# Performance work log

Measured on AMD Instinct MI355X. Metric: run time of the kernel, lower is better.

The kernel has to match this reference:

```python
import jax, jax.numpy as jnp
import numpy as np

B, S, D, H, BU = 64, 1024, 256, 512, 512  # batch, seq_len, input_size, units, backbone width


def setup_inputs() -> dict:
    key = jax.random.key(0)
    k0, k1, k2, k3 = jax.random.split(key, 4)
    inputs = jax.random.normal(k0, (B, S, D), dtype=jnp.float32)
    # backbone: Linear(D+H -> BU) (single layer, no trailing activation per build_backbone)
    Wb = jax.random.normal(k1, (D + H, BU), dtype=jnp.float32) * 0.02
    bb = jnp.zeros((BU,), dtype=jnp.float32)
    # head: Linear(BU -> H)
    Wh = jax.random.normal(k2, (BU, H), dtype=jnp.float32) * 0.02
    bh = jnp.zeros((H,), dtype=jnp.float32)
    # per-unit liquid time constant tau > 0
    tau = 1.0 + jax.random.uniform(k3, (H,), dtype=jnp.float32)
    return {"inputs": inputs, "Wb": Wb, "bb": bb, "Wh": Wh, "bh": bh, "tau": tau}


def reference(inputs, Wb, bb, Wh, bh, tau):
    # LiquidRNN: unidirectional, return_sequences=True, zero initial state, dt=1.0
    dt = jnp.float32(1.0)
    batch = inputs.shape[0]
    h0 = jnp.zeros((batch, Wh.shape[1]), dtype=inputs.dtype)

    def step(h, x):  # x: [B, D], h: [B, H]
        z = jnp.concatenate([x, h], axis=-1) @ Wb + bb          # backbone [B, BU]
        d = jnp.tanh(z @ Wh + bh)                               # target activation [B, H]
        h_new = h + dt * (d - h) / tau                          # liquid ODE (Euler) update
        return h_new, h_new

    _, outs = jax.lax.scan(step, h0, jnp.swapaxes(inputs, 0, 1))  # outs: [S, B, H]
    return jnp.swapaxes(outs, 0, 1)  # [B, S, H]
```

## Files before the change

### kernel.cpp

```cpp
#include <hip/hip_runtime.h>
#include <hip/hip_bf16.h>


#define S_   1024
#define D_   256
#define H_   512
#define KT_  768
#define NKC_ 24

typedef __attribute__((ext_vector_type(4))) float f32x4;
typedef __attribute__((ext_vector_type(8))) short bf16x8;
typedef unsigned long long u64;

static __device__ __forceinline__ unsigned short f2bf(float f) {
    unsigned int x = __float_as_uint(f);
    return (unsigned short)((x + 0x7fffu + ((x >> 16) & 1u)) >> 16);
}

__global__ void k_prep(const float* __restrict__ Wb, const float* __restrict__ bb,
                       const float* __restrict__ Wh, const float* __restrict__ bh,
                       const float* __restrict__ tau,
                       unsigned short* __restrict__ Mfrag, float* __restrict__ c,
                       float* __restrict__ itau, unsigned* __restrict__ hz) {
    int i = blockIdx.x * 256 + threadIdx.x;
    if (i < KT_ * H_) {
        int r = i >> 9, n = i & 511;
        float acc = 0.f;
        for (int u = 0; u < 512; ++u)
            acc += Wb[r * 512 + u] * Wh[u * 512 + n];
        int kc   = r >> 5;
        int j    = r & 7;
        int lane = (((r >> 3) & 3) << 4) | (n & 15);
        int nt   = n >> 4;
        Mfrag[((nt * NKC_ + kc) * 64 + lane) * 8 + j] = f2bf(acc);
    } else if (i < KT_ * H_ + 512) {
        int n = i - KT_ * H_;
        float acc = bh[n];
        for (int u = 0; u < 512; ++u)
            acc += bb[u] * Wh[u * 512 + n];
        c[n] = acc;
    } else if (i < KT_ * H_ + 1024) {
        itau[i - KT_ * H_ - 512] = 1.0f / tau[i - KT_ * H_ - 512];
    } else {
        int z = i - KT_ * H_ - 1024;
        if (z < 65536) hz[z] = 0u;
    }
}

__global__ __launch_bounds__(256, 1)
void k_rnn2(const float* __restrict__ x, const unsigned short* __restrict__ Mfrag,
            const float* __restrict__ c, const float* __restrict__ itau,
            u64* __restrict__ hb, float* __restrict__ out) {
    const int g    = blockIdx.x >> 3;
    const int s    = blockIdx.x & 7;
    const int tid  = threadIdx.x;
    const int w    = tid >> 6;
    const int lane = tid & 63;
    const int quad = lane >> 4;
    const int m16  = lane & 15;
    const int nt   = s * 4 + w;
    const int C0   = nt * 16 + quad * 4;
    const int b    = g * 16 + m16;

    const bf16x8* Mf = reinterpret_cast<const bf16x8*>(Mfrag);
    bf16x8 wreg[NKC_];
#pragma unroll
    for (int kc = 0; kc < NKC_; ++kc)
        wreg[kc] = Mf[(nt * NKC_ + kc) * 64 + lane];

    const f32x4 cs = *reinterpret_cast<const f32x4*>(c + C0);
    const f32x4 ts = *reinterpret_cast<const f32x4*>(itau + C0);

    const int jsel = quad & 1;
    const int st_u = ((C0 >> 3) * 16 + m16) * 4 + jsel * 2;
    const int ld_u = lane * 4;

    f32x4 h_old = {0.f, 0.f, 0.f, 0.f};

    for (int t = 0; t < S_; ++t) {
        const float* xp = x + ((size_t)b * S_ + t) * D_ + quad * 8;
        f32x4 xa[8], xb[8];
#pragma unroll
        for (int kc = 0; kc < 8; ++kc) {
            xa[kc] = *reinterpret_cast<const f32x4*>(xp + kc * 32);
            xb[kc] = *reinterpret_cast<const f32x4*>(xp + kc * 32 + 4);
        }
        f32x4 a0 = {0.f, 0.f, 0.f, 0.f}, a1 = {0.f, 0.f, 0.f, 0.f};
#pragma unroll
        for (int kc = 0; kc < 8; ++kc) {
            bf16x8 xv;
#pragma unroll
            for (int j = 0; j < 4; ++j) {
                xv[j]     = (short)f2bf(xa[kc][j]);
                xv[j + 4] = (short)f2bf(xb[kc][j]);
            }
            if (kc & 1) a1 = __builtin_amdgcn_mfma_f32_16x16x32_bf16(wreg[kc], xv, a1, 0, 0, 0);
            else        a0 = __builtin_amdgcn_mfma_f32_16x16x32_bf16(wreg[kc], xv, a0, 0, 0, 0);
        }

        if (t > 0) {
            u64* hbl = hb + (size_t)(g * 2 + (t & 1)) * 4096;
            u64 hl[16][4];
#pragma unroll
            for (int kc = 0; kc < 16; ++kc) {
#pragma unroll
                for (int q = 0; q < 4; ++q)
                    hl[kc][q] = __hip_atomic_load(hbl + kc * 256 + ld_u + q,
                                                  __ATOMIC_RELAXED, __HIP_MEMORY_SCOPE_AGENT);
            }
            const unsigned T = (unsigned)t << 16;
            for (;;) {
                unsigned bad = 0u;
#pragma unroll
                for (int kc = 0; kc < 16; ++kc) {
#pragma unroll
                    for (int q = 0; q < 4; ++q) {
                        unsigned lo = (unsigned)hl[kc][q];
                        unsigned hi = (unsigned)(hl[kc][q] >> 32);
                        bad |= (lo ^ T) | (hi ^ T);
                    }
                }
                if (!__any((bad & 0xFFFF0000u) != 0u)) break;
#pragma unroll
                for (int kc = 0; kc < 16; ++kc) {
#pragma unroll
                    for (int q = 0; q < 4; ++q)
                        hl[kc][q] = __hip_atomic_load(hbl + kc * 256 + ld_u + q,
                                                      __ATOMIC_RELAXED, __HIP_MEMORY_SCOPE_AGENT);
                }
            }
#pragma unroll
            for (int kc = 0; kc < 16; ++kc) {
                union { unsigned wv[4]; bf16x8 v; } hv;
#pragma unroll
                for (int q = 0; q < 4; ++q) {
                    unsigned lo = (unsigned)hl[kc][q];
                    unsigned hi = (unsigned)(hl[kc][q] >> 32);
                    hv.wv[q] = (lo & 0xffffu) | (hi << 16);
                }
                if (kc & 1) a1 = __builtin_amdgcn_mfma_f32_16x16x32_bf16(wreg[8 + kc], hv.v, a1, 0, 0, 0);
                else        a0 = __builtin_amdgcn_mfma_f32_16x16x32_bf16(wreg[8 + kc], hv.v, a0, 0, 0, 0);
            }
        }

        f32x4 acc = a0 + a1;
        f32x4 hn;
        unsigned dv[4];
        const unsigned Tn = (unsigned)(t + 1) << 16;
#pragma unroll
        for (int r = 0; r < 4; ++r) {
            float u = acc[r] + cs[r];
            float e = __expf(2.f * u);
            float d = 1.f - 2.f / (e + 1.f);
            hn[r] = h_old[r] + (d - h_old[r]) * ts[r];
            dv[r] = (unsigned)f2bf(hn[r]) | Tn;
        }
        h_old = hn;

        u64 p0 = (u64)dv[0] | ((u64)dv[1] << 32);
        u64 p1 = (u64)dv[2] | ((u64)dv[3] << 32);
        u64* hbs = hb + (size_t)(g * 2 + ((t + 1) & 1)) * 4096;
        __hip_atomic_store(hbs + st_u,     p0, __ATOMIC_RELAXED, __HIP_MEMORY_SCOPE_AGENT);
        __hip_atomic_store(hbs + st_u + 1, p1, __ATOMIC_RELAXED, __HIP_MEMORY_SCOPE_AGENT);

        *reinterpret_cast<f32x4*>(out + ((size_t)b * S_ + t) * H_ + C0) = hn;
    }
}

extern "C" void kernel_launch(void* const* d_in, const int* in_sizes, int n_in,
                              void* d_out, int out_size, void* d_ws, size_t ws_size,
                              hipStream_t stream) {
    const float* x   = (const float*)d_in[0];
    const float* Wb  = (const float*)d_in[1];
    const float* bb  = (const float*)d_in[2];
    const float* Wh  = (const float*)d_in[3];
    const float* bh  = (const float*)d_in[4];
    const float* tau = (const float*)d_in[5];
    float* out = (float*)d_out;

    char* ws = (char*)d_ws;
    unsigned short* Mfrag = (unsigned short*)ws;
    float*          c     = (float*)(ws + 786432);
    float*          it    = (float*)(ws + 788480);
    u64*            hbuf  = (u64*)(ws + 790528);

    hipLaunchKernelGGL(k_prep, dim3(1796), dim3(256), 0, stream,
                       Wb, bb, Wh, bh, tau, Mfrag, c, it, (unsigned*)hbuf);
    hipLaunchKernelGGL(k_rnn2, dim3(32), dim3(256), 0, stream,
                       x, Mfrag, c, it, hbuf, out);
}
```

Measured before the change: 6.044 ms.

## Add per-block step flags, prefetch next-step inputs, and widen MFMA accumulator chains

Consumers now spin on eight per-group step counters, written by each block after a vmcnt drain and a block barrier, before they load the tagged hidden-state buffer. The old spin kept re-reading all 64 words per lane. The next timestep's x is prefetched and converted to bf16 with packed cvt instructions off the critical path. The recurrent MFMA chain is split across four accumulators, and unpacking uses v_perm. The extra __syncthreads and waitcnt per step add latency on the serial chain.

```diff
diff --git a/kernel.cpp b/kernel.cpp
--- a/kernel.cpp
+++ b/kernel.cpp
@@ -11,6 +11,7 @@
 typedef __attribute__((ext_vector_type(4))) float f32x4;
 typedef __attribute__((ext_vector_type(8))) short bf16x8;
 typedef unsigned long long u64;
+typedef unsigned int u32;
 
 static __device__ __forceinline__ unsigned short f2bf(float f) {
     unsigned int x = __float_as_uint(f);
@@ -21,7 +22,7 @@
                        const float* __restrict__ Wh, const float* __restrict__ bh,
                        const float* __restrict__ tau,
                        unsigned short* __restrict__ Mfrag, float* __restrict__ c,
-                       float* __restrict__ itau, unsigned* __restrict__ hz) {
+                       float* __restrict__ itau, u32* __restrict__ hz) {
     int i = blockIdx.x * 256 + threadIdx.x;
     if (i < KT_ * H_) {
         int r = i >> 9, n = i & 511;
@@ -43,14 +44,14 @@
         itau[i - KT_ * H_ - 512] = 1.0f / tau[i - KT_ * H_ - 512];
     } else {
         int z = i - KT_ * H_ - 1024;
-        if (z < 65536) hz[z] = 0u;
+        if (z < 65536 + 64) hz[z] = 0u;
     }
 }
 
 __global__ __launch_bounds__(256, 1)
 void k_rnn2(const float* __restrict__ x, const unsigned short* __restrict__ Mfrag,
             const float* __restrict__ c, const float* __restrict__ itau,
-            u64* __restrict__ hb, float* __restrict__ out) {
+            u64* __restrict__ hb, u32* __restrict__ fl, float* __restrict__ out) {
     const int g    = blockIdx.x >> 3;
     const int s    = blockIdx.x & 7;
     const int tid  = threadIdx.x;
@@ -74,33 +75,49 @@
     const int jsel = quad & 1;
     const int st_u = ((C0 >> 3) * 16 + m16) * 4 + jsel * 2;
     const int ld_u = lane * 4;
+    u64* flq = reinterpret_cast<u64*>(fl) + g * 8;
+
+    f32x4 xr[16];
+    {
+        const float* xq = x + (size_t)b * (S_ * D_) + quad * 8;
+#pragma unroll
+        for (int kc = 0; kc < 8; ++kc) {
+            xr[2 * kc]     = *reinterpret_cast<const f32x4*>(xq + kc * 32);
+            xr[2 * kc + 1] = *reinterpret_cast<const f32x4*>(xq + kc * 32 + 4);
+        }
+    }
+    bf16x8 xv[8];
+#pragma unroll
+    for (int kc = 0; kc < 8; ++kc) {
+        union { u32 u[4]; bf16x8 v; } t_;
+#pragma unroll
+        for (int j = 0; j < 4; ++j) {
+            float lo = (j < 2) ? xr[2 * kc][2 * j]     : xr[2 * kc + 1][2 * j - 4];
+            float hi = (j < 2) ? xr[2 * kc][2 * j + 1] : xr[2 * kc + 1][2 * j - 3];
+            asm("v_cvt_pk_bf16_f32 %0, %1, %2" : "=v"(t_.u[j]) : "v"(lo), "v"(hi));
+        }
+        xv[kc] = t_.v;
+    }
 
     f32x4 h_old = {0.f, 0.f, 0.f, 0.f};
 
     for (int t = 0; t < S_; ++t) {
-        const float* xp = x + ((size_t)b * S_ + t) * D_ + quad * 8;
-        f32x4 xa[8], xb[8];
-#pragma unroll
-        for (int kc = 0; kc < 8; ++kc) {
-            xa[kc] = *reinterpret_cast<const f32x4*>(xp + kc * 32);
-            xb[kc] = *reinterpret_cast<const f32x4*>(xp + kc * 32 + 4);
-        }
-        f32x4 a0 = {0.f, 0.f, 0.f, 0.f}, a1 = {0.f, 0.f, 0.f, 0.f};
-#pragma unroll
-        for (int kc = 0; kc < 8; ++kc) {
-            bf16x8 xv;
-#pragma unroll
-            for (int j = 0; j < 4; ++j) {
-                xv[j]     = (short)f2bf(xa[kc][j]);
-                xv[j + 4] = (short)f2bf(xb[kc][j]);
-            }
-            if (kc & 1) a1 = __builtin_amdgcn_mfma_f32_16x16x32_bf16(wreg[kc], xv, a1, 0, 0, 0);
-            else        a0 = __builtin_amdgcn_mfma_f32_16x16x32_bf16(wreg[kc], xv, a0, 0, 0, 0);
-        }
+        u64 hl[16][4];
+        u64* hbl = hb + (size_t)(g * 2 + (t & 1)) * 4096;
 
         if (t > 0) {
-            u64* hbl = hb + (size_t)(g * 2 + (t & 1)) * 4096;
-            u64 hl[16][4];
+            for (;;) {
+                u64 f0 = __hip_atomic_load(flq + 0, __ATOMIC_RELAXED, __HIP_MEMORY_SCOPE_AGENT);
+                u64 f1 = __hip_atomic_load(flq + 1, __ATOMIC_RELAXED, __HIP_MEMORY_SCOPE_AGENT);
+                u64 f2 = __hip_atomic_load(flq + 2, __ATOMIC_RELAXED, __HIP_MEMORY_SCOPE_AGENT);
+                u64 f3 = __hip_atomic_load(flq + 3, __ATOMIC_RELAXED, __HIP_MEMORY_SCOPE_AGENT);
+                u32 m = (u32)f0;
+                m = min(m, (u32)(f0 >> 32));
+                m = min(m, (u32)f1); m = min(m, (u32)(f1 >> 32));
+                m = min(m, (u32)f2); m = min(m, (u32)(f2 >> 32));
+                m = min(m, (u32)f3); m = min(m, (u32)(f3 >> 32));
+                if (m >= (u32)t) break;
+            }
 #pragma unroll
             for (int kc = 0; kc < 16; ++kc) {
 #pragma unroll
@@ -108,19 +125,37 @@
                     hl[kc][q] = __hip_atomic_load(hbl + kc * 256 + ld_u + q,
                                                   __ATOMIC_RELAXED, __HIP_MEMORY_SCOPE_AGENT);
             }
-            const unsigned T = (unsigned)t << 16;
+        }
+
+        {
+            int tn = (t + 1) & (S_ - 1);
+            const float* xq = x + ((size_t)b * S_ + tn) * D_ + quad * 8;
+#pragma unroll
+            for (int kc = 0; kc < 8; ++kc) {
+                xr[2 * kc]     = *reinterpret_cast<const f32x4*>(xq + kc * 32);
+                xr[2 * kc + 1] = *reinterpret_cast<const f32x4*>(xq + kc * 32 + 4);
+            }
+        }
+
+        f32x4 aA = {0.f, 0.f, 0.f, 0.f}, aB = aA, aC = aA, aD = aA;
+#pragma unroll
+        for (int kc = 0; kc < 8; ++kc) {
+            if (kc & 1) aB = __builtin_amdgcn_mfma_f32_16x16x32_bf16(wreg[kc], xv[kc], aB, 0, 0, 0);
+            else        aA = __builtin_amdgcn_mfma_f32_16x16x32_bf16(wreg[kc], xv[kc], aA, 0, 0, 0);
+        }
+
+        if (t > 0) {
+            const u64 TT = ((u64)(u32)t << 48) | ((u64)(u32)t << 16);
             for (;;) {
-                unsigned bad = 0u;
+                u64 bad = 0;
 #pragma unroll
                 for (int kc = 0; kc < 16; ++kc) {
 #pragma unroll
-                    for (int q = 0; q < 4; ++q) {
-                        unsigned lo = (unsigned)hl[kc][q];
-                        unsigned hi = (unsigned)(hl[kc][q] >> 32);
-                        bad |= (lo ^ T) | (hi ^ T);
-                    }
+                    for (int q = 0; q < 4; ++q)
+                        bad |= (hl[kc][q] ^ TT);
                 }
-                if (!__any((bad & 0xFFFF0000u) != 0u)) break;
+                bad &= 0xFFFF0000FFFF0000ull;
+                if (!__any(bad != 0ull)) break;
 #pragma unroll
                 for (int kc = 0; kc < 16; ++kc) {
 #pragma unroll
@@ -131,29 +166,31 @@
             }
 #pragma unroll
             for (int kc = 0; kc < 16; ++kc) {
-                union { unsigned wv[4]; bf16x8 v; } hv;
-#pragma unroll
-                for (int q = 0; q < 4; ++q) {
-                    unsigned lo = (unsigned)hl[kc][q];
-                    unsigned hi = (unsigned)(hl[kc][q] >> 32);
-                    hv.wv[q] = (lo & 0xffffu) | (hi << 16);
+                union { u32 u[4]; bf16x8 v; } hv;
+#pragma unroll
+                for (int q = 0; q < 4; ++q)
+                    hv.u[q] = __builtin_amdgcn_perm((u32)(hl[kc][q] >> 32),
+                                                    (u32)hl[kc][q], 0x05040100u);
+                switch (kc & 3) {
+                    case 0: aA = __builtin_amdgcn_mfma_f32_16x16x32_bf16(wreg[8 + kc], hv.v, aA, 0, 0, 0); break;
+                    case 1: aB = __builtin_amdgcn_mfma_f32_16x16x32_bf16(wreg[8 + kc], hv.v, aB, 0, 0, 0); break;
+                    case 2: aC = __builtin_amdgcn_mfma_f32_16x16x32_bf16(wreg[8 + kc], hv.v, aC, 0, 0, 0); break;
+                    default: aD = __builtin_amdgcn_mfma_f32_16x16x32_bf16(wreg[8 + kc], hv.v, aD, 0, 0, 0); break;
                 }
-                if (kc & 1) a1 = __builtin_amdgcn_mfma_f32_16x16x32_bf16(wreg[8 + kc], hv.v, a1, 0, 0, 0);
-                else        a0 = __builtin_amdgcn_mfma_f32_16x16x32_bf16(wreg[8 + kc], hv.v, a0, 0, 0, 0);
-            }
-        }
-
-        f32x4 acc = a0 + a1;
+            }
+        }
+
+        f32x4 acc = (aA + aB) + (aC + aD);
         f32x4 hn;
-        unsigned dv[4];
-        const unsigned Tn = (unsigned)(t + 1) << 16;
+        u32 dv[4];
+        const u32 Tn = (u32)(t + 1) << 16;
 #pragma unroll
         for (int r = 0; r < 4; ++r) {
             float u = acc[r] + cs[r];
             float e = __expf(2.f * u);
             float d = 1.f - 2.f / (e + 1.f);
             hn[r] = h_old[r] + (d - h_old[r]) * ts[r];
-            dv[r] = (unsigned)f2bf(hn[r]) | Tn;
+            dv[r] = (u32)f2bf(hn[r]) | Tn;
         }
         h_old = hn;
 
@@ -163,7 +200,25 @@
         __hip_atomic_store(hbs + st_u,     p0, __ATOMIC_RELAXED, __HIP_MEMORY_SCOPE_AGENT);
         __hip_atomic_store(hbs + st_u + 1, p1, __ATOMIC_RELAXED, __HIP_MEMORY_SCOPE_AGENT);
 
+        asm volatile("s_waitcnt vmcnt(0)" ::: "memory");
+        __syncthreads();
+        if (tid == 0)
+            __hip_atomic_store(fl + g * 16 + s, (u32)(t + 1),
+                               __ATOMIC_RELAXED, __HIP_MEMORY_SCOPE_AGENT);
+
         *reinterpret_cast<f32x4*>(out + ((size_t)b * S_ + t) * H_ + C0) = hn;
+
+#pragma unroll
+        for (int kc = 0; kc < 8; ++kc) {
+            union { u32 u[4]; bf16x8 v; } t_;
+#pragma unroll
+            for (int j = 0; j < 4; ++j) {
+                float lo = (j < 2) ? xr[2 * kc][2 * j]     : xr[2 * kc + 1][2 * j - 4];
+                float hi = (j < 2) ? xr[2 * kc][2 * j + 1] : xr[2 * kc + 1][2 * j - 3];
+                asm("v_cvt_pk_bf16_f32 %0, %1, %2" : "=v"(t_.u[j]) : "v"(lo), "v"(hi));
+            }
+            xv[kc] = t_.v;
+        }
     }
 }
 
@@ -183,9 +238,10 @@
     float*          c     = (float*)(ws + 786432);
     float*          it    = (float*)(ws + 788480);
     u64*            hbuf  = (u64*)(ws + 790528);
-
-    hipLaunchKernelGGL(k_prep, dim3(1796), dim3(256), 0, stream,
-                       Wb, bb, Wh, bh, tau, Mfrag, c, it, (unsigned*)hbuf);
+    u32*            flags = (u32*)(ws + 1052672);
+
+    hipLaunchKernelGGL(k_prep, dim3(1797), dim3(256), 0, stream,
+                       Wb, bb, Wh, bh, tau, Mfrag, c, it, (u32*)hbuf);
     hipLaunchKernelGGL(k_rnn2, dim3(32), dim3(256), 0, stream,
-                       x, Mfrag, c, it, hbuf, out);
-}
+                       x, Mfrag, c, it, hbuf, flags, out);
+}
```

Measured after the change: 10.16 ms. 1.68x slower.
